# Optimization experiments

Measured on AMD Instinct MI355X. Metric: run time of the kernel, lower is better.

The kernel has to match this reference:

```python
import jax, jax.numpy as jnp
import numpy as np

N_PKG, N_TGT, E = 20000, 30000, 100000
NT, IN, H, C1 = 6, 400, 4, 64   # 6 edge types, in_channels, heads, conv1 out per head
D1 = H * C1                     # 256 = out_channels * num_heads
K = 128                         # diffpool clusters per node type
C2 = 64                         # conv2 (hidden_channels) per head


def gatv2_sparse(x_s, x_t, src, tgt, Ws, Wt, att, slope=0.2):
    """Bipartite GATv2Conv: per-edge LeakyReLU scores, segment softmax over target
    neighborhoods, weighted scatter-aggregate. Returns [n_tgt, H*C]."""
    n_t = x_t.shape[0]
    h, c = att.shape
    l = (x_s @ Ws).reshape(x_s.shape[0], h, c)   # [Ns,H,C]
    r = (x_t @ Wt).reshape(n_t, h, c)            # [Nt,H,C]
    le, re = l[src], r[tgt]                      # [E,H,C] gathers
    e = jnp.einsum('ehc,hc->eh', jax.nn.leaky_relu(le + re, slope), att)  # [E,H]
    emax = jax.ops.segment_max(e, tgt, num_segments=n_t)
    emax = jnp.where(jnp.isfinite(emax), emax, 0.0)
    ex = jnp.exp(e - emax[tgt])
    den = jax.ops.segment_sum(ex, tgt, num_segments=n_t)
    alpha = ex / (den[tgt] + 1e-16)
    out = jax.ops.segment_sum(le * alpha[..., None], tgt, num_segments=n_t)
    return out.reshape(n_t, h * c)


def gatv2_dense_attn(p_s, p_t, A, Ws, Wt, att, slope=0.2):
    """GATv2 attention over the dense pooled bipartite graph; returns alpha [Ks,Kt,H]."""
    h, c = att.shape
    l = (p_s @ Ws).reshape(-1, h, c)
    r = (p_t @ Wt).reshape(-1, h, c)
    e = jnp.einsum('ijhc,hc->ijh', jax.nn.leaky_relu(l[:, None] + r[None, :], slope), att)
    e = jnp.where(A[..., None] > 0, e, -1e9)
    return jax.nn.softmax(e, axis=0)  # softmax over source clusters


def setup_inputs() -> dict:
    key = jax.random.key(0)
    ks = jax.random.split(key, 14)
    p = 0.05
    return {
        'x_pkg': jax.random.normal(ks[0], (N_PKG, IN), jnp.float32),
        'x_tgt': jax.random.normal(ks[1], (NT, N_TGT, IN), jnp.float32),
        'src_idx': jax.random.randint(ks[2], (NT, E), 0, N_PKG),
        'tgt_idx': jax.random.randint(ks[3], (NT, E), 0, N_TGT),
        'W1s': jax.random.normal(ks[4], (NT, IN, D1), jnp.float32) * p,
        'W1t': jax.random.normal(ks[5], (NT, IN, D1), jnp.float32) * p,
        'a1': jax.random.normal(ks[6], (NT, H, C1), jnp.float32) * p,
        'Wpkg': jax.random.normal(ks[7], (IN, D1), jnp.float32) * p,
        'Wassign': jax.random.normal(ks[8], (NT + 1, D1, K), jnp.float32) * p,
        'W2s': jax.random.normal(ks[9], (NT, D1, D1), jnp.float32) * p,
        'W2t': jax.random.normal(ks[10], (NT, D1, D1), jnp.float32) * p,
        'a2': jax.random.normal(ks[11], (NT, H, C2), jnp.float32) * p,
        'Wcls': jax.random.normal(ks[12], (D1, 1), jnp.float32) * p,
        'bcls': jnp.zeros((1,), jnp.float32),
    }


def reference(x_pkg, x_tgt, src_idx, tgt_idx, W1s, W1t, a1, Wpkg, Wassign,
              W2s, W2t, a2, Wcls, bcls):
    nt = x_tgt.shape[0]
    n_pkg, n_tgt = x_pkg.shape[0], x_tgt.shape[1]
    n_edges = jnp.float32(src_idx.shape[1])

    # --- conv1: heterogeneous GATv2 per edge type, then ReLU ---
    h_tgt = [jax.nn.relu(gatv2_sparse(x_pkg, x_tgt[t], src_idx[t], tgt_idx[t],
                                      W1s[t], W1t[t], a1[t])) for t in range(nt)]
    h_pkg = jax.nn.relu(x_pkg @ Wpkg)  # HeteroGNN embedding for source type

    # --- diffpool: soft cluster assignments, pooled features, losses ---
    S_pkg = jax.nn.softmax(h_pkg @ Wassign[0], axis=-1)            # [N_pkg,K]
    S_tgt = [jax.nn.softmax(h_tgt[t] @ Wassign[t + 1], axis=-1) for t in range(nt)]
    p_pkg = S_pkg.T @ h_pkg                                        # [K,D1]
    p_tgt = [S_tgt[t].T @ h_tgt[t] for t in range(nt)]

    def ent(S):
        return jnp.mean(-jnp.sum(S * jnp.log(S + 1e-15), axis=-1))
    ent_loss = ent(S_pkg) + sum(ent(S) for S in S_tgt)

    M_pkg = S_pkg.T @ S_pkg                                        # [K,K]
    link_loss = jnp.float32(0.0)
    attn2 = []
    for t in range(nt):
        Ss = S_pkg[src_idx[t]]                                     # [E,K]
        St = S_tgt[t][tgt_idx[t]]                                  # [E,K]
        A_pool = jnp.einsum('ek,el->kl', Ss, St)                   # pooled adjacency [K,K]
        # ||A - S_src S_tgt^T||_F without materializing dense A:
        dot = jnp.sum(Ss * St)
        Mt = S_tgt[t].T @ S_tgt[t]
        norm2 = n_edges - 2.0 * dot + jnp.sum(M_pkg * Mt)
        link_loss = link_loss + jnp.sqrt(jax.nn.relu(norm2) + 1e-12) / float(n_pkg * n_tgt)
        # --- conv2: GATv2 attention over pooled dense graph ---
        attn2.append(gatv2_dense_attn(p_pkg, p_tgt[t], A_pool, W2s[t], W2t[t], a2[t]))

    # --- classifier over all pooled nodes ---
    all_pooled = jnp.concatenate([p_pkg] + p_tgt, axis=0)          # [(NT+1)*K, D1]
    probs = jax.nn.sigmoid(all_pooled @ Wcls + bcls)               # [(NT+1)*K, 1]
    return probs, link_loss + ent_loss, jnp.stack(attn2)           # attn: [NT,K,K,H]
```

## Files before the change

### kernel.cpp

```cpp
#include <hip/hip_runtime.h>
#include <math.h>

#define NPKG   20000
#define NTGT   30000
#define NEDGE  100000
#define NTYPES 6
#define INDIM  400
#define KP_IN  416
#define MP_PKG 20096
#define MP_TGT 30080

#define LSTR   ((size_t)MP_PKG * 256)
#define RSTR   ((size_t)MP_TGT * 256)
#define XSTR   ((size_t)MP_TGT * KP_IN)
#define LOGSTR ((size_t)MP_TGT * 128)
#define SSTR   ((size_t)MP_TGT * 128)
#define WSTR   ((size_t)256 * KP_IN)

typedef unsigned short ushortT;
typedef unsigned int uintT;
typedef __attribute__((ext_vector_type(8))) short bf16x8;
typedef __attribute__((ext_vector_type(8))) short short8b;
typedef __attribute__((ext_vector_type(4))) float f32x4;

__device__ __forceinline__ float lrelu(float x) { return x > 0.f ? x : 0.2f * x; }
__device__ __forceinline__ float b2f(ushortT u) {
  union { unsigned int i; float f; } x; x.i = ((unsigned int)u) << 16; return x.f;
}
__device__ __forceinline__ ushortT f2b(float f) {
  unsigned int u = __float_as_uint(f);
  unsigned int r = (u + 0x7FFFu + ((u >> 16) & 1u)) >> 16;
  return (ushortT)r;
}

#define GLL16(g, l)                                                            \
  __builtin_amdgcn_global_load_lds(                                            \
      (const __attribute__((address_space(1))) void*)(g),                      \
      (__attribute__((address_space(3))) void*)(l), 16, 0, 0)

__global__ void zero_f32(float* __restrict__ p, long n) {
  long i = blockIdx.x * 256 + threadIdx.x, st = (long)gridDim.x * 256;
  for (; i < n; i += st) p[i] = 0.f;
}

__global__ void zero_tails(ushortT* __restrict__ S_all, ushortT* __restrict__ h_t) {
  int t = blockIdx.y;
  int i = blockIdx.x * 256 + threadIdx.x;
  ushort4 z = {0, 0, 0, 0};
  if (i < 2560) {
    int r = i >> 5, c = (i & 31) * 4;
    *(ushort4*)(S_all + (size_t)t * SSTR + (size_t)(30000 + r) * 128 + c) = z;
  } else if (i < 7680) {
    int k = i - 2560;
    int r = k >> 6, c = (k & 63) * 4;
    *(ushort4*)(h_t + (size_t)t * RSTR + (size_t)(30000 + r) * 256 + c) = z;
  }
}

__global__ void convert_pad(const float* __restrict__ src, ushortT* __restrict__ dst,
                            int M, int K, int Kp, long srcStride, long dstStride) {
  long z = blockIdx.y;
  const float* s = src + z * srcStride;
  ushortT* d = dst + z * dstStride;
  int idx = blockIdx.x * 256 + threadIdx.x;
  int q = Kp >> 2;
  int row = idx / q, c4 = (idx - row * q) * 4;
  if (row >= M) return;
  float4 v = make_float4(0.f, 0.f, 0.f, 0.f);
  if (c4 < K) v = *(const float4*)(s + (size_t)row * K + c4);
  ushort4 o;
  o.x = f2b(v.x); o.y = f2b(v.y); o.z = f2b(v.z); o.w = f2b(v.w);
  *(ushort4*)(d + (size_t)row * Kp + c4) = o;
}

__global__ void wtrans13(const float* __restrict__ W1s, const float* __restrict__ Wpkg,
                         const float* __restrict__ W1t, ushortT* __restrict__ WT) {
  int z = blockIdx.y;
  const float* Wb = (z < 6) ? (W1s + (size_t)z * INDIM * 256)
                  : (z == 6) ? Wpkg
                  : (W1t + (size_t)(z - 7) * INDIM * 256);
  ushortT* WTb = WT + (size_t)z * WSTR;
  int idx = blockIdx.x * 256 + threadIdx.x;
  if (idx >= 256 * KP_IN) return;
  int n = idx / KP_IN, k = idx - n * KP_IN;
  WTb[idx] = (k < INDIM) ? f2b(Wb[(size_t)k * 256 + n]) : (ushortT)0;
}

__global__ void wtransAss(const float* __restrict__ W, ushortT* __restrict__ WT) {
  int z = blockIdx.y;
  const float* Wb = W + (size_t)z * 256 * 128;
  ushortT* WTb = WT + (size_t)z * 128 * 256;
  int idx = blockIdx.x * 256 + threadIdx.x;
  if (idx >= 128 * 256) return;
  int n = idx >> 8, k = idx & 255;
  WTb[idx] = f2b(Wb[(size_t)k * 128 + n]);
}

struct MfmaBatch {
  const ushortT* A[8];
  const ushortT* BT[8];
  void* C[8];
  int M[8];
  int relu[8];
};

template<bool WF32>
__global__ __launch_bounds__(256) void gemm_mfma_b(MfmaBatch d, int Kp, int N) {
  const int z = blockIdx.z;
  const int M = d.M[z];
  const int m0 = blockIdx.y * 128;
  if (m0 >= M) return;
  const ushortT* A = d.A[z];
  const ushortT* BT = d.BT[z];
  const int relu = d.relu[z];
  __shared__ ushortT As[128 * 32];
  __shared__ ushortT Bs[128 * 32];
  const int tid = threadIdx.x;
  const int wave = tid >> 6, lane = tid & 63;
  const int lr = lane & 15, hk = lane >> 4;
  const int am = (wave >> 1) * 64;
  const int bn = (wave & 1) * 64;
  const int n0 = blockIdx.x * 128;

  const int row1 = tid >> 2, cg = (tid & 3) * 8;
  const int row2 = row1 + 64;
  ushortT* ldsA1 = As + ((tid >> 6) << 9);
  ushortT* ldsA2 = As + 2048 + ((tid >> 6) << 9);
  ushortT* ldsB1 = Bs + ((tid >> 6) << 9);
  ushortT* ldsB2 = Bs + 2048 + ((tid >> 6) << 9);
  const ushortT* gA1 = A + (size_t)(m0 + row1) * Kp + cg;
  const ushortT* gA2 = A + (size_t)(m0 + row2) * Kp + cg;
  const ushortT* gB1 = BT + (size_t)(n0 + row1) * Kp + cg;
  const ushortT* gB2 = BT + (size_t)(n0 + row2) * Kp + cg;

  f32x4 acc[4][4];
#pragma unroll
  for (int i = 0; i < 4; ++i)
#pragma unroll
    for (int j = 0; j < 4; ++j) acc[i][j] = (f32x4)(0.f);

  const int nk = Kp >> 5;
  for (int kt = 0; kt < nk; ++kt) {
    const int k0 = kt << 5;
    GLL16(gA1 + k0, ldsA1);
    GLL16(gA2 + k0, ldsA2);
    GLL16(gB1 + k0, ldsB1);
    GLL16(gB2 + k0, ldsB2);
    __syncthreads();
    bf16x8 af[4], bfr[4];
#pragma unroll
    for (int i = 0; i < 4; ++i)
      af[i] = *(const bf16x8*)(As + (size_t)(am + i * 16 + lr) * 32 + hk * 8);
#pragma unroll
    for (int j = 0; j < 4; ++j)
      bfr[j] = *(const bf16x8*)(Bs + (size_t)(bn + j * 16 + lr) * 32 + hk * 8);
#pragma unroll
    for (int i = 0; i < 4; ++i)
#pragma unroll
      for (int j = 0; j < 4; ++j)
        acc[i][j] = __builtin_amdgcn_mfma_f32_16x16x32_bf16(af[i], bfr[j], acc[i][j], 0, 0, 0);
    __syncthreads();
  }

#pragma unroll
  for (int i = 0; i < 4; ++i) {
#pragma unroll
    for (int reg = 0; reg < 4; ++reg) {
      int row = m0 + am + i * 16 + hk * 4 + reg;
      if (row < M) {
#pragma unroll
        for (int j = 0; j < 4; ++j) {
          int col = n0 + bn + j * 16 + lr;
          float v = acc[i][j][reg];
          if (relu) v = fmaxf(v, 0.f);
          if (WF32) ((float*)d.C[z])[(size_t)row * N + col] = v;
          else      ((ushortT*)d.C[z])[(size_t)row * N + col] = f2b(v);
        }
      }
    }
  }
}

struct TnBatch {
  const ushortT* A[8];
  const ushortT* B[8];
  float* C[8];
  const int* rA[8];
  const int* rB[8];
  int N[8];
};

template<int K2>
__global__ __launch_bounds__(256) void gemm_tn_mfma(TnBatch d, int chunk, int nchunk) {
  const int mat = blockIdx.z / nchunk;
  const int ci = blockIdx.z - mat * nchunk;
  const int N = d.N[mat];
  const int kbeg = ci * chunk;
  if (kbeg >= N) return;
  const int kend = min(N, kbeg + chunk);
  const ushortT* __restrict__ A = d.A[mat];
  const ushortT* __restrict__ B = d.B[mat];
  const int* __restrict__ rA = d.rA[mat];
  const int* __restrict__ rB = d.rB[mat];
  float* __restrict__ C = d.C[mat];
  const int n0 = (K2 == 256) ? blockIdx.x * 128 : 0;

  __shared__ uintT AtU[2048];
  __shared__ uintT BtU[2048];
  const ushortT* At = (const ushortT*)AtU;
  const ushortT* Bt = (const ushortT*)BtU;

  const int tid = threadIdx.x;
  const int kp = tid >> 4;
  const int mo8 = tid & 15;
  const int mh = mo8 >> 1;
  const int mlo = (mo8 & 1) * 8;
  const uintT wbase = (uintT)mh * 256 + (uintT)(kp >> 2) * 64 + (uintT)(kp & 3);
  const int wave = tid >> 6, lane = tid & 63;
  const int lr = lane & 15, hk = lane >> 4;
  const int wm = wave >> 1, wn = wave & 1;
  int offA[4], offB[4];
#pragma unroll
  for (int i = 0; i < 4; ++i) {
    int Rm = wm * 4 + i, Rn = wn * 4 + i;
    offA[i] = Rm * 512 + hk * 128 + (lr ^ Rm) * 8;
    offB[i] = Rn * 512 + hk * 128 + (lr ^ Rn) * 8;
  }

  f32x4 acc[4][4];
#pragma unroll
  for (int i = 0; i < 4; ++i)
#pragma unroll
    for (int j = 0; j < 4; ++j) acc[i][j] = (f32x4)(0.f);

  for (int k0 = kbeg; k0 < kend; k0 += 32) {
    const int r0 = k0 + kp * 2;
    int ia0, ia1, ib0, ib1;
    if (rA) { int2 v = *(const int2*)(rA + r0); ia0 = v.x; ia1 = v.y; }
    else    { ia0 = r0; ia1 = r0 + 1; }
    if (rB) { int2 v = *(const int2*)(rB + r0); ib0 = v.x; ib1 = v.y; }
    else    { ib0 = r0; ib1 = r0 + 1; }
    bf16x8 a0 = *(const bf16x8*)(A + (size_t)ia0 * 128 + mo8 * 8);
    bf16x8 a1 = *(const bf16x8*)(A + (size_t)ia1 * 128 + mo8 * 8);
    bf16x8 b0, b1;
    if (K2 == 256) {
      b0 = *(const bf16x8*)(B + (size_t)ib0 * 256 + n0 + mo8 * 8);
      b1 = *(const bf16x8*)(B + (size_t)ib1 * 256 + n0 + mo8 * 8);
    } else {
      b0 = *(const bf16x8*)(B + (size_t)ib0 * 128 + mo8 * 8);
      b1 = *(const bf16x8*)(B + (size_t)ib1 * 128 + mo8 * 8);
    }
#pragma unroll
    for (int j = 0; j < 8; ++j) {
      uintT off = wbase + (uintT)((mlo + j) ^ mh) * 4;
      AtU[off] = (uintT)(ushortT)a0[j] | ((uintT)(ushortT)a1[j] << 16);
      BtU[off] = (uintT)(ushortT)b0[j] | ((uintT)(ushortT)b1[j] << 16);
    }
    __syncthreads();
    bf16x8 af[4], bfr[4];
#pragma unroll
    for (int i = 0; i < 4; ++i) af[i] = *(const bf16x8*)(At + offA[i]);
#pragma unroll
    for (int j = 0; j < 4; ++j) bfr[j] = *(const bf16x8*)(Bt + offB[j]);
#pragma unroll
    for (int i = 0; i < 4; ++i)
#pragma unroll
      for (int j = 0; j < 4; ++j)
        acc[i][j] = __builtin_amdgcn_mfma_f32_16x16x32_bf16(af[i], bfr[j], acc[i][j], 0, 0, 0);
    __syncthreads();
  }

#pragma unroll
  for (int i = 0; i < 4; ++i) {
    int mbase = wm * 64 + i * 16 + hk * 4;
#pragma unroll
    for (int reg = 0; reg < 4; ++reg) {
#pragma unroll
      for (int j = 0; j < 4; ++j) {
        int n = n0 + wn * 64 + j * 16 + lr;
        atomicAdd(&C[(size_t)(mbase + reg) * K2 + n], acc[i][j][reg]);
      }
    }
  }
}

__global__ void hist_kernel(const int* __restrict__ tgt, int* __restrict__ counts,
                            int nE, int ntgt) {
  int t = blockIdx.y;
  int e = blockIdx.x * 256 + threadIdx.x;
  if (e < nE) atomicAdd(&counts[t * ntgt + tgt[(long)t * nE + e]], 1);
}

__global__ __launch_bounds__(1024) void scan_kernel(const int* __restrict__ counts_all,
                                                    int* __restrict__ offs_all,
                                                    int* __restrict__ cursor_all, int n) {
  __shared__ int lsum[1024];
  int ty = blockIdx.x;
  const int* counts = counts_all + (long)ty * n;
  int* offs = offs_all + (long)ty * (n + 1);
  int* cursor = cursor_all + (long)ty * n;
  int t = threadIdx.x;
  int chunk = (n + 1023) >> 10;
  int base = t * chunk;
  int s = 0;
  for (int i = 0; i < chunk; ++i) {
    int idx = base + i;
    if (idx < n) s += counts[idx];
  }
  lsum[t] = s;
  __syncthreads();
  for (int off = 1; off < 1024; off <<= 1) {
    int v = (t >= off) ? lsum[t - off] : 0;
    __syncthreads();
    lsum[t] += v;
    __syncthreads();
  }
  int run = lsum[t] - s;
  for (int i = 0; i < chunk; ++i) {
    int idx = base + i;
    if (idx < n) {
      offs[idx] = run;
      cursor[idx] = run;
      run += counts[idx];
    }
  }
  if (t == 1023) offs[n] = lsum[1023];
}

__global__ void scatter_kernel(const int* __restrict__ tgt, int* __restrict__ cursor,
                               int* __restrict__ eorder, int nE, int ntgt) {
  int t = blockIdx.y;
  int e = blockIdx.x * 256 + threadIdx.x;
  if (e < nE) {
    int tv = tgt[(long)t * nE + e];
    int p = atomicAdd(&cursor[t * ntgt + tv], 1);
    eorder[(long)t * nE + p] = e;
  }
}

__global__ __launch_bounds__(256) void conv1_agg(const ushortT* __restrict__ l_all,
                                                 const ushortT* __restrict__ r_all,
                                                 const float* __restrict__ a1,
                                                 const int* __restrict__ src_all,
                                                 const int* __restrict__ eorder_all,
                                                 const int* __restrict__ offs_all,
                                                 ushortT* __restrict__ h_all) {
  int t = blockIdx.y;
  const ushortT* l = l_all + (size_t)t * LSTR;
  const ushortT* r = r_all + (size_t)t * RSTR;
  const float* a1t = a1 + t * 256;
  const int* src = src_all + (long)t * NEDGE;
  const int* eorder = eorder_all + (long)t * NEDGE;
  const int* offs = offs_all + (long)t * (NTGT + 1);
  ushortT* hout = h_all + (size_t)t * RSTR;

  int wid = threadIdx.x >> 6, lane = threadIdx.x & 63;
  int v = blockIdx.x * 4 + wid;
  if (v >= NTGT) return;
  ushort4 ru = *(const ushort4*)(r + (size_t)v * 256 + lane * 4);
  float rx = b2f(ru.x), ry = b2f(ru.y), rz = b2f(ru.z), rw = b2f(ru.w);
  const float4 aa = *(const float4*)(a1t + lane * 4);
  int beg = offs[v], end = offs[v + 1];
  float ax = 0.f, ay = 0.f, az = 0.f, aw = 0.f, den = 0.f;
  for (int p = beg; p < end; ++p) {
    int e = eorder[p];
    int u = src[e];
    ushort4 lu = *(const ushort4*)(l + (size_t)u * 256 + lane * 4);
    float lx = b2f(lu.x), ly = b2f(lu.y), lz = b2f(lu.z), lw = b2f(lu.w);
    float s = lrelu(lx + rx) * aa.x + lrelu(ly + ry) * aa.y +
              lrelu(lz + rz) * aa.z + lrelu(lw + rw) * aa.w;
#pragma unroll
    for (int m = 1; m < 16; m <<= 1) s += __shfl_xor(s, m, 64);
    float w = expf(s);
    ax += w * lx; ay += w * ly; az += w * lz; aw += w * lw;
    den += w;
  }
  float inv = (end > beg) ? 1.f / den : 0.f;
  ushort4 o;
  o.x = f2b(fmaxf(ax * inv, 0.f));
  o.y = f2b(fmaxf(ay * inv, 0.f));
  o.z = f2b(fmaxf(az * inv, 0.f));
  o.w = f2b(fmaxf(aw * inv, 0.f));
  *(ushort4*)(hout + (size_t)v * 256 + lane * 4) = o;
}

__global__ __launch_bounds__(256) void softmax_ent(const float* __restrict__ logits_all,
                                                   ushortT* __restrict__ S_all,
                                                   float* __restrict__ ent_slots) {
  int z = blockIdx.y;
  int nrows = (z == 6) ? NPKG : NTGT;
  if (blockIdx.x * 32 >= nrows) return;
  float inv_n = 1.f / (float)nrows;
  const float* logits = logits_all + (size_t)z * LOGSTR;
  ushortT* Sb = S_all + (size_t)z * SSTR;

  int wid = threadIdx.x >> 6, lane = threadIdx.x & 63;
  int rloc = lane >> 3, seg = lane & 7;
  int v = blockIdx.x * 32 + wid * 8 + rloc;
  bool valid = v < nrows;

  const float* row = logits + (size_t)v * 128 + seg * 16;
  f32x4 x0 = *(const f32x4*)(row);
  f32x4 x1 = *(const f32x4*)(row + 4);
  f32x4 x2 = *(const f32x4*)(row + 8);
  f32x4 x3 = *(const f32x4*)(row + 12);

  float m01 = fmaxf(fmaxf(x0.x, x0.y), fmaxf(x0.z, x0.w));
  float m11 = fmaxf(fmaxf(x1.x, x1.y), fmaxf(x1.z, x1.w));
  float m21 = fmaxf(fmaxf(x2.x, x2.y), fmaxf(x2.z, x2.w));
  float m31 = fmaxf(fmaxf(x3.x, x3.y), fmaxf(x3.z, x3.w));
  float m = fmaxf(fmaxf(m01, m11), fmaxf(m21, m31));
#pragma unroll
  for (int sh = 1; sh < 8; sh <<= 1) m = fmaxf(m, __shfl_xor(m, sh, 64));

  f32x4 e0, e1, e2, e3;
  float s = 0.f, tt = 0.f;
#pragma unroll
  for (int q = 0; q < 4; ++q) {
    f32x4 xq = (q == 0) ? x0 : (q == 1) ? x1 : (q == 2) ? x2 : x3;
    f32x4 eq;
#pragma unroll
    for (int c = 0; c < 4; ++c) {
      float d = xq[c] - m;
      float e = expf(d);
      eq[c] = e;
      s += e;
      tt += e * d;
    }
    if (q == 0) e0 = eq; else if (q == 1) e1 = eq; else if (q == 2) e2 = eq; else e3 = eq;
  }
#pragma unroll
  for (int sh = 1; sh < 8; sh <<= 1) {
    s += __shfl_xor(s, sh, 64);
    tt += __shfl_xor(tt, sh, 64);
  }
  float inv = 1.f / s;

  if (valid) {
    short8b lo, hi;
#pragma unroll
    for (int c = 0; c < 4; ++c) {
      lo[c]     = (short)f2b(e0[c] * inv);
      lo[c + 4] = (short)f2b(e1[c] * inv);
      hi[c]     = (short)f2b(e2[c] * inv);
      hi[c + 4] = (short)f2b(e3[c] * inv);
    }
    ushortT* op = Sb + (size_t)v * 128 + seg * 16;
    *(short8b*)(op) = lo;
    *(short8b*)(op + 8) = hi;
  }

  float val = (valid && seg == 0) ? (logf(s) - tt / s) * inv_n : 0.f;
#pragma unroll
  for (int sh = 1; sh < 64; sh <<= 1) val += __shfl_xor(val, sh, 64);
  if (lane == 0) atomicAdd(&ent_slots[blockIdx.x & 255], val);
}

__global__ __launch_bounds__(256) void link_kernel(const float* __restrict__ Apool_all,
                                                   const float* __restrict__ M_all,
                                                   float Ef, float scale,
                                                   float* __restrict__ loss) {
  __shared__ float red[256];
  int ty = blockIdx.x;
  const float* Apool = Apool_all + (size_t)ty * 16384;
  const float* Mp = M_all + (size_t)6 * 16384;
  const float* Mt = M_all + (size_t)ty * 16384;
  int t = threadIdx.x;
  float s = 0.f;
  for (int i = t; i < 16384; i += 256) s += Mp[i] * Mt[i];
  if (t < 128) s -= 2.f * Apool[t * 129];
  red[t] = s;
  __syncthreads();
  for (int sh = 128; sh > 0; sh >>= 1) {
    if (t < sh) red[t] += red[t + sh];
    __syncthreads();
  }
  if (t == 0) {
    float norm2 = Ef + red[0];
    atomicAdd(loss, sqrtf(fmaxf(norm2, 0.f) + 1e-12f) * scale);
  }
}

__global__ __launch_bounds__(256) void conv2_gemm(const float* __restrict__ p_buf,
                                                  const float* __restrict__ W2s,
                                                  const float* __restrict__ W2t,
                                                  float* __restrict__ l2r2) {
  const int z = blockIdx.z;
  const int sel = z / 6, t = z - sel * 6;
  const float* A = p_buf + (sel ? (size_t)(t + 1) * 32768 : 0);
  const float* B = (sel ? W2t : W2s) + (size_t)t * 65536;
  float* C = l2r2 + (size_t)sel * 196608 + (size_t)t * 32768;
  const int M = 128, K = 256, N = 256;
  __shared__ __align__(16) float As[16][136];
  __shared__ __align__(16) float Bs[16][136];
  const int tid = threadIdx.x;
  const int tx = tid & 15, ty = tid >> 4;
  const int n0 = blockIdx.x * 128;
  float acc[8][8];
#pragma unroll
  for (int i = 0; i < 8; ++i)
#pragma unroll
    for (int j = 0; j < 8; ++j) acc[i][j] = 0.f;
  for (int k0 = 0; k0 < K; k0 += 16) {
#pragma unroll
    for (int i = 0; i < 8; ++i) {
      int idx = tid + i * 256;
      int rr = idx >> 4, kk = idx & 15;
      As[kk][rr] = (rr < M) ? A[(size_t)rr * K + (k0 + kk)] : 0.f;
    }
#pragma unroll
    for (int i = 0; i < 8; ++i) {
      int idx = tid + i * 256;
      int kk = idx >> 7, nn = idx & 127;
      Bs[kk][nn] = B[(size_t)(k0 + kk) * N + (n0 + nn)];
    }
    __syncthreads();
#pragma unroll
    for (int kk = 0; kk < 16; ++kk) {
      float4 a0 = *(const float4*)&As[kk][ty * 8];
      float4 a1 = *(const float4*)&As[kk][ty * 8 + 4];
      float4 b0 = *(const float4*)&Bs[kk][tx * 8];
      float4 b1 = *(const float4*)&Bs[kk][tx * 8 + 4];
      float av[8] = {a0.x, a0.y, a0.z, a0.w, a1.x, a1.y, a1.z, a1.w};
      float bv[8] = {b0.x, b0.y, b0.z, b0.w, b1.x, b1.y, b1.z, b1.w};
#pragma unroll
      for (int i = 0; i < 8; ++i)
#pragma unroll
        for (int j = 0; j < 8; ++j) acc[i][j] += av[i] * bv[j];
    }
    __syncthreads();
  }
#pragma unroll
  for (int i = 0; i < 8; ++i) {
    int m = ty * 8 + i;
    if (m < M) {
#pragma unroll
      for (int j = 0; j < 8; ++j)
        C[(size_t)m * N + n0 + tx * 8 + j] = acc[i][j];
    }
  }
}

__global__ __launch_bounds__(256) void conv2_attn(const float* __restrict__ l2_all,
                                                  const float* __restrict__ r2_all,
                                                  const float* __restrict__ Apool_all,
                                                  const float* __restrict__ a2_all,
                                                  float* __restrict__ attn_out) {
  __shared__ float r2row[256], a2s[256], sc[512];
  int j = blockIdx.x;
  int t = blockIdx.y;
  int tid = threadIdx.x;
  const float* l2 = l2_all + (long)t * 32768;
  const float* Apool = Apool_all + (long)t * 16384;
  r2row[tid] = r2_all[(long)t * 32768 + j * 256 + tid];
  a2s[tid] = a2_all[t * 256 + tid];
  __syncthreads();
#pragma unroll
  for (int p = tid; p < 512; p += 256) {
    int i = p >> 2, h = p & 3;
    const float* lr_ = l2 + i * 256 + h * 64;
    const float* rr_ = r2row + h * 64;
    const float* av_ = a2s + h * 64;
    float s = 0.f;
    for (int c = 0; c < 64; ++c) {
      float x = lr_[c] + rr_[c];
      s += (x > 0.f ? x : 0.2f * x) * av_[c];
    }
    sc[p] = (Apool[i * 128 + j] > 0.f) ? s : -1e9f;
  }
  __syncthreads();
  int h = tid >> 6, lane = tid & 63;
  float v0 = sc[lane * 4 + h], v1 = sc[(lane + 64) * 4 + h];
  float m = fmaxf(v0, v1);
#pragma unroll
  for (int sh = 1; sh < 64; sh <<= 1) m = fmaxf(m, __shfl_xor(m, sh, 64));
  float e0 = expf(v0 - m), e1 = expf(v1 - m);
  float s = e0 + e1;
#pragma unroll
  for (int sh = 1; sh < 64; sh <<= 1) s += __shfl_xor(s, sh, 64);
  float inv = 1.f / s;
  attn_out[(long)t * 65536 + (long)lane * 512 + j * 4 + h] = e0 * inv;
  attn_out[(long)t * 65536 + (long)(lane + 64) * 512 + j * 4 + h] = e1 * inv;
}

__global__ __launch_bounds__(256) void classifier(const float* __restrict__ p_all,
                                                  const float* __restrict__ Wcls,
                                                  const float* __restrict__ bcls,
                                                  float* __restrict__ out, int nrows) {
  int wid = threadIdx.x >> 6, lane = threadIdx.x & 63;
  int rrow = blockIdx.x * 4 + wid;
  if (rrow >= nrows) return;
  const float4 w = *(const float4*)(Wcls + lane * 4);
  const float4 x = *(const float4*)(p_all + (long)rrow * 256 + lane * 4);
  float s = x.x * w.x + x.y * w.y + x.z * w.z + x.w * w.w;
#pragma unroll
  for (int sh = 1; sh < 64; sh <<= 1) s += __shfl_xor(s, sh, 64);
  if (lane == 0) out[rrow] = 1.f / (1.f + expf(-(s + bcls[0])));
}

__global__ void finalize_loss(const float* __restrict__ red_buf, float* __restrict__ out896) {
  __shared__ float red[256];
  int t = threadIdx.x;
  red[t] = red_buf[t];
  __syncthreads();
  for (int sh = 128; sh > 0; sh >>= 1) {
    if (t < sh) red[t] += red[t + sh];
    __syncthreads();
  }
  if (t == 0) out896[0] = red[0] + red_buf[256];
}

extern "C" void kernel_launch(void* const* d_in, const int* in_sizes, int n_in,
                              void* d_out, int out_size, void* d_ws, size_t ws_size,
                              hipStream_t stream) {
  (void)in_sizes; (void)n_in; (void)out_size; (void)ws_size;
  const float* x_pkg  = (const float*)d_in[0];
  const float* x_tgt  = (const float*)d_in[1];
  const int* src_idx  = (const int*)d_in[2];
  const int* tgt_idx  = (const int*)d_in[3];
  const float* W1s    = (const float*)d_in[4];
  const float* W1t    = (const float*)d_in[5];
  const float* a1     = (const float*)d_in[6];
  const float* Wpkg   = (const float*)d_in[7];
  const float* Wassign= (const float*)d_in[8];
  const float* W2s    = (const float*)d_in[9];
  const float* W2t    = (const float*)d_in[10];
  const float* a2     = (const float*)d_in[11];
  const float* Wcls   = (const float*)d_in[12];
  const float* bcls   = (const float*)d_in[13];
  float* out = (float*)d_out;

  char* wp = (char*)d_ws;
  auto alloc = [&](size_t bytes) -> char* {
    char* r = wp;
    wp += (bytes + 255) & ~(size_t)255;
    return r;
  };
  float* p_buf   = (float*)alloc((size_t)7 * 32768 * 4);
  float* M_all   = (float*)alloc((size_t)7 * 16384 * 4);
  float* Apool   = (float*)alloc((size_t)NTYPES * 16384 * 4);
  float* red_buf = (float*)alloc(257 * 4);
  int* counts    = (int*)alloc((size_t)NTYPES * NTGT * 4);
  long zero_n = ((char*)counts + (size_t)NTYPES * NTGT * 4 - (char*)p_buf) / 4;
  int* offs      = (int*)alloc((size_t)NTYPES * (NTGT + 1) * 4);
  int* cursor    = (int*)alloc((size_t)NTYPES * NTGT * 4);
  int* eorder    = (int*)alloc((size_t)NTYPES * NEDGE * 4);
  ushortT* x_pkg_bf = (ushortT*)alloc((size_t)MP_PKG * KP_IN * 2);
  ushortT* x_t_bf   = (ushortT*)alloc((size_t)NTYPES * XSTR * 2);
  ushortT* WT_all   = (ushortT*)alloc((size_t)13 * WSTR * 2);
  ushortT* WassT    = (ushortT*)alloc((size_t)7 * 128 * 256 * 2);
  ushortT* h_pkg_bf = (ushortT*)alloc((size_t)MP_PKG * 256 * 2);
  ushortT* l_bf     = (ushortT*)alloc((size_t)NTYPES * LSTR * 2);
  ushortT* r_bf     = (ushortT*)alloc((size_t)NTYPES * RSTR * 2);
  ushortT* h_t_bf   = (ushortT*)alloc((size_t)NTYPES * RSTR * 2);
  float* logits     = (float*)alloc((size_t)7 * LOGSTR * 4);
  ushortT* S_all    = (ushortT*)alloc((size_t)7 * SSTR * 2);
  float* l2r2       = (float*)alloc((size_t)12 * 32768 * 4);
  float* ent_slots  = red_buf;
  float* loss_acc   = red_buf + 256;
  float* l2_all = l2r2;
  float* r2_all = l2r2 + (size_t)6 * 32768;

  dim3 blk(256);

  zero_f32<<<dim3(512), blk, 0, stream>>>(p_buf, zero_n);
  zero_tails<<<dim3(30, NTYPES), blk, 0, stream>>>(S_all, h_t_bf);

  convert_pad<<<dim3((NPKG * (KP_IN / 4) + 255) / 256, 1), blk, 0, stream>>>(
      x_pkg, x_pkg_bf, NPKG, INDIM, KP_IN, 0, 0);
  convert_pad<<<dim3((NTGT * (KP_IN / 4) + 255) / 256, NTYPES), blk, 0, stream>>>(
      x_tgt, x_t_bf, NTGT, INDIM, KP_IN, (long)NTGT * INDIM, (long)XSTR);

  wtrans13<<<dim3((256 * KP_IN + 255) / 256, 13), blk, 0, stream>>>(W1s, Wpkg, W1t, WT_all);
  wtransAss<<<dim3((128 * 256 + 255) / 256, 7), blk, 0, stream>>>(Wassign, WassT);

  hist_kernel<<<dim3(391, NTYPES), blk, 0, stream>>>(tgt_idx, counts, NEDGE, NTGT);
  scan_kernel<<<dim3(NTYPES), dim3(1024), 0, stream>>>(counts, offs, cursor, NTGT);
  scatter_kernel<<<dim3(391, NTYPES), blk, 0, stream>>>(tgt_idx, cursor, eorder, NEDGE, NTGT);

  {
    MfmaBatch d{};
    for (int z = 0; z < 6; ++z) {
      d.A[z] = x_pkg_bf; d.BT[z] = WT_all + (size_t)z * WSTR;
      d.C[z] = l_bf + (size_t)z * LSTR; d.M[z] = NPKG; d.relu[z] = 0;
    }
    d.A[6] = x_pkg_bf; d.BT[6] = WT_all + (size_t)6 * WSTR;
    d.C[6] = h_pkg_bf; d.M[6] = NPKG; d.relu[6] = 1;
    d.A[7] = d.A[0]; d.BT[7] = d.BT[0]; d.C[7] = d.C[0]; d.M[7] = 0; d.relu[7] = 0;
    gemm_mfma_b<false><<<dim3(2, 157, 7), blk, 0, stream>>>(d, KP_IN, 256);
  }

  {
    MfmaBatch d{};
    for (int z = 0; z < 6; ++z) {
      d.A[z] = x_t_bf + (size_t)z * XSTR; d.BT[z] = WT_all + (size_t)(7 + z) * WSTR;
      d.C[z] = r_bf + (size_t)z * RSTR; d.M[z] = NTGT; d.relu[z] = 0;
    }
    for (int z = 6; z < 8; ++z) { d.A[z] = d.A[0]; d.BT[z] = d.BT[0]; d.C[z] = d.C[0]; d.M[z] = 0; d.relu[z] = 0; }
    gemm_mfma_b<false><<<dim3(2, 235, 6), blk, 0, stream>>>(d, KP_IN, 256);
  }

  conv1_agg<<<dim3(7500, NTYPES), blk, 0, stream>>>(l_bf, r_bf, a1, src_idx, eorder, offs, h_t_bf);

  {
    MfmaBatch d{};
    for (int z = 0; z < 6; ++z) {
      d.A[z] = h_t_bf + (size_t)z * RSTR; d.BT[z] = WassT + (size_t)(z + 1) * 128 * 256;
      d.C[z] = logits + (size_t)z * LOGSTR; d.M[z] = NTGT; d.relu[z] = 0;
    }
    d.A[6] = h_pkg_bf; d.BT[6] = WassT; d.C[6] = logits + (size_t)6 * LOGSTR;
    d.M[6] = NPKG; d.relu[6] = 0;
    d.A[7] = d.A[0]; d.BT[7] = d.BT[0]; d.C[7] = d.C[0]; d.M[7] = 0; d.relu[7] = 0;
    gemm_mfma_b<true><<<dim3(1, 235, 7), blk, 0, stream>>>(d, 256, 128);
  }

  softmax_ent<<<dim3(938, 7), blk, 0, stream>>>(logits, S_all, ent_slots);

  {
    TnBatch d{};
    for (int m = 0; m < 6; ++m) {
      d.A[m] = S_all + (size_t)m * SSTR; d.B[m] = h_t_bf + (size_t)m * RSTR;
      d.C[m] = p_buf + (size_t)(m + 1) * 32768;
      d.rA[m] = nullptr; d.rB[m] = nullptr; d.N[m] = MP_TGT;
    }
    d.A[6] = S_all + (size_t)6 * SSTR; d.B[6] = h_pkg_bf; d.C[6] = p_buf;
    d.rA[6] = nullptr; d.rB[6] = nullptr; d.N[6] = NPKG;
    d.A[7] = d.A[0]; d.B[7] = d.B[0]; d.C[7] = d.C[0]; d.rA[7] = nullptr; d.rB[7] = nullptr; d.N[7] = 0;
    gemm_tn_mfma<256><<<dim3(2, 1, 7 * 30), blk, 0, stream>>>(d, 1024, 30);
  }

  {
    TnBatch d{};
    for (int m = 0; m < 7; ++m) {
      const ushortT* S = S_all + (size_t)m * SSTR;
      d.A[m] = S; d.B[m] = S; d.C[m] = M_all + (size_t)m * 16384;
      d.rA[m] = nullptr; d.rB[m] = nullptr; d.N[m] = (m == 6) ? NPKG : MP_TGT;
    }
    d.A[7] = d.A[0]; d.B[7] = d.B[0]; d.C[7] = d.C[0]; d.rA[7] = nullptr; d.rB[7] = nullptr; d.N[7] = 0;
    gemm_tn_mfma<128><<<dim3(1, 1, 7 * 30), blk, 0, stream>>>(d, 1024, 30);
  }

  {
    TnBatch d{};
    for (int m = 0; m < 6; ++m) {
      d.A[m] = S_all + (size_t)6 * SSTR; d.B[m] = S_all + (size_t)m * SSTR;
      d.C[m] = Apool + (size_t)m * 16384;
      d.rA[m] = src_idx + (long)m * NEDGE; d.rB[m] = tgt_idx + (long)m * NEDGE;
      d.N[m] = NEDGE;
    }
    for (int m = 6; m < 8; ++m) { d.A[m] = d.A[0]; d.B[m] = d.B[0]; d.C[m] = d.C[0]; d.rA[m] = nullptr; d.rB[m] = nullptr; d.N[m] = 0; }
    gemm_tn_mfma<128><<<dim3(1, 1, 6 * 98), blk, 0, stream>>>(d, 1024, 98);
  }

  link_kernel<<<dim3(6), blk, 0, stream>>>(Apool, M_all, (float)NEDGE,
                                           1.f / ((float)NPKG * (float)NTGT), loss_acc);

  conv2_gemm<<<dim3(2, 1, 12), blk, 0, stream>>>(p_buf, W2s, W2t, l2r2);
  conv2_attn<<<dim3(128, NTYPES), blk, 0, stream>>>(l2_all, r2_all, Apool, a2, out + 897);

  classifier<<<dim3(224), blk, 0, stream>>>(p_buf, Wcls, bcls, out, 896);
  finalize_loss<<<dim3(1), blk, 0, stream>>>(red_buf, out + 896);
}
```

Before: 1.274 ms.

## Store sorted source indices in CSR and prefetch neighbor rows in conv1 aggregation

The scatter kernel now writes the source node id directly into the CSR edge array instead of the edge id, so the aggregation loop no longer does two dependent index loads per edge. In conv1_agg, each wave loads up to 64 neighbor indices at once, broadcasts them with shuffles, and software-prefetches the next neighbor's feature row while computing the current one. This shortens the chain of dependent global loads per edge, at the cost of a few extra shuffles and an extra read of src_idx in the scatter kernel.

```diff
diff --git a/kernel.cpp b/kernel.cpp
--- a/kernel.cpp
+++ b/kernel.cpp
@@ -327,30 +327,29 @@
   if (t == 1023) offs[n] = lsum[1023];
 }
 
-__global__ void scatter_kernel(const int* __restrict__ tgt, int* __restrict__ cursor,
-                               int* __restrict__ eorder, int nE, int ntgt) {
+__global__ void scatter_kernel(const int* __restrict__ tgt, const int* __restrict__ src,
+                               int* __restrict__ cursor, int* __restrict__ srcs,
+                               int nE, int ntgt) {
   int t = blockIdx.y;
   int e = blockIdx.x * 256 + threadIdx.x;
   if (e < nE) {
     int tv = tgt[(long)t * nE + e];
     int p = atomicAdd(&cursor[t * ntgt + tv], 1);
-    eorder[(long)t * nE + p] = e;
+    srcs[(long)t * nE + p] = src[(long)t * nE + e];
   }
 }
 
 __global__ __launch_bounds__(256) void conv1_agg(const ushortT* __restrict__ l_all,
                                                  const ushortT* __restrict__ r_all,
                                                  const float* __restrict__ a1,
-                                                 const int* __restrict__ src_all,
-                                                 const int* __restrict__ eorder_all,
+                                                 const int* __restrict__ srcs_all,
                                                  const int* __restrict__ offs_all,
                                                  ushortT* __restrict__ h_all) {
   int t = blockIdx.y;
   const ushortT* l = l_all + (size_t)t * LSTR;
   const ushortT* r = r_all + (size_t)t * RSTR;
   const float* a1t = a1 + t * 256;
-  const int* src = src_all + (long)t * NEDGE;
-  const int* eorder = eorder_all + (long)t * NEDGE;
+  const int* srcs = srcs_all + (long)t * NEDGE;
   const int* offs = offs_all + (long)t * (NTGT + 1);
   ushortT* hout = h_all + (size_t)t * RSTR;
 
@@ -362,18 +361,27 @@
   const float4 aa = *(const float4*)(a1t + lane * 4);
   int beg = offs[v], end = offs[v + 1];
   float ax = 0.f, ay = 0.f, az = 0.f, aw = 0.f, den = 0.f;
-  for (int p = beg; p < end; ++p) {
-    int e = eorder[p];
-    int u = src[e];
-    ushort4 lu = *(const ushort4*)(l + (size_t)u * 256 + lane * 4);
-    float lx = b2f(lu.x), ly = b2f(lu.y), lz = b2f(lu.z), lw = b2f(lu.w);
-    float s = lrelu(lx + rx) * aa.x + lrelu(ly + ry) * aa.y +
-              lrelu(lz + rz) * aa.z + lrelu(lw + rw) * aa.w;
-#pragma unroll
-    for (int m = 1; m < 16; m <<= 1) s += __shfl_xor(s, m, 64);
-    float w = expf(s);
-    ax += w * lx; ay += w * ly; az += w * lz; aw += w * lw;
-    den += w;
+
+  for (int cbeg = beg; cbeg < end; cbeg += 64) {
+    int cnt = min(64, end - cbeg);
+    int sidx = (lane < cnt) ? srcs[cbeg + lane] : 0;
+    int u0 = __shfl(sidx, 0, 64);
+    ushort4 lu = *(const ushort4*)(l + (size_t)u0 * 256 + lane * 4);
+    for (int q = 0; q < cnt; ++q) {
+      ushort4 cur = lu;
+      if (q + 1 < cnt) {
+        int un = __shfl(sidx, q + 1, 64);
+        lu = *(const ushort4*)(l + (size_t)un * 256 + lane * 4);
+      }
+      float lx = b2f(cur.x), ly = b2f(cur.y), lz = b2f(cur.z), lw = b2f(cur.w);
+      float s = lrelu(lx + rx) * aa.x + lrelu(ly + ry) * aa.y +
+                lrelu(lz + rz) * aa.z + lrelu(lw + rw) * aa.w;
+#pragma unroll
+      for (int m = 1; m < 16; m <<= 1) s += __shfl_xor(s, m, 64);
+      float w = expf(s);
+      ax += w * lx; ay += w * ly; az += w * lz; aw += w * lw;
+      den += w;
+    }
   }
   float inv = (end > beg) ? 1.f / den : 0.f;
   ushort4 o;
@@ -644,7 +652,7 @@
   long zero_n = ((char*)counts + (size_t)NTYPES * NTGT * 4 - (char*)p_buf) / 4;
   int* offs      = (int*)alloc((size_t)NTYPES * (NTGT + 1) * 4);
   int* cursor    = (int*)alloc((size_t)NTYPES * NTGT * 4);
-  int* eorder    = (int*)alloc((size_t)NTYPES * NEDGE * 4);
+  int* srcs      = (int*)alloc((size_t)NTYPES * NEDGE * 4);
   ushortT* x_pkg_bf = (ushortT*)alloc((size_t)MP_PKG * KP_IN * 2);
   ushortT* x_t_bf   = (ushortT*)alloc((size_t)NTYPES * XSTR * 2);
   ushortT* WT_all   = (ushortT*)alloc((size_t)13 * WSTR * 2);
@@ -676,7 +684,7 @@
 
   hist_kernel<<<dim3(391, NTYPES), blk, 0, stream>>>(tgt_idx, counts, NEDGE, NTGT);
   scan_kernel<<<dim3(NTYPES), dim3(1024), 0, stream>>>(counts, offs, cursor, NTGT);
-  scatter_kernel<<<dim3(391, NTYPES), blk, 0, stream>>>(tgt_idx, cursor, eorder, NEDGE, NTGT);
+  scatter_kernel<<<dim3(391, NTYPES), blk, 0, stream>>>(tgt_idx, src_idx, cursor, srcs, NEDGE, NTGT);
 
   {
     MfmaBatch d{};
@@ -700,7 +708,7 @@
     gemm_mfma_b<false><<<dim3(2, 235, 6), blk, 0, stream>>>(d, KP_IN, 256);
   }
 
-  conv1_agg<<<dim3(7500, NTYPES), blk, 0, stream>>>(l_bf, r_bf, a1, src_idx, eorder, offs, h_t_bf);
+  conv1_agg<<<dim3(7500, NTYPES), blk, 0, stream>>>(l_bf, r_bf, a1, srcs, offs, h_t_bf);
 
   {
     MfmaBatch d{};
```

New measurement: 1.238 ms. 1.03x faster.
